# Kernel tuning notes

Hardware: AMD Instinct MI355X
Metric: run time of the kernel (lower is better)

Reference implementation:

```python
import jax, jax.numpy as jnp
import numpy as np

B, S, H, F, E, K = 2, 2048, 1024, 4096, 8, 2


def setup_inputs() -> dict:
    key = jax.random.key(0)
    ks = jax.random.split(key, 5)
    scale = 0.02
    return {
        "hidden_states": jax.random.normal(ks[0], (B, S, H), jnp.float32),
        "gate_w": jax.random.normal(ks[1], (H, E), jnp.float32) * scale,  # nn.Linear(H,E,bias=False)
        "w1": jax.random.normal(ks[2], (E, H, F), jnp.float32) * scale,   # per-expert fc1
        "b1": jnp.zeros((E, F), jnp.float32),
        "w2": jax.random.normal(ks[3], (E, F, H), jnp.float32) * scale,   # per-expert fc2
        "b2": jnp.zeros((E, H), jnp.float32),
    }


def reference(hidden_states, gate_w, w1, b1, w2, b2):
    b, s, h = hidden_states.shape
    x = hidden_states.reshape(b * s, h)  # [T, H]
    T = x.shape[0]
    n_experts = gate_w.shape[1]

    # --- Top-K gating ---
    router_logits = x @ gate_w                      # [T, E]
    router_probs = jax.nn.softmax(router_logits, axis=-1)
    topk_probs, topk_idx = jax.lax.top_k(router_probs, K)  # [T, K]
    topk_probs = topk_probs / topk_probs.sum(axis=-1, keepdims=True)
    aux_loss = n_experts * jnp.sum(router_probs.mean(axis=0) ** 2)

    # --- Combine weights: scatter normalized top-k probs into dense [T, E] ---
    combine_w = jnp.zeros((T, n_experts), x.dtype).at[
        jnp.arange(T)[:, None], topk_idx
    ].add(topk_probs)

    # --- Expert MLPs (dense per-expert batched GEMM; zero combine weight drops unrouted) ---
    hidden = jax.nn.relu(jnp.einsum('th,ehf->etf', x, w1) + b1[:, None, :])  # [E, T, F]
    expert_out = jnp.einsum('etf,efh->eth', hidden, w2) + b2[:, None, :]     # [E, T, H]

    out = jnp.einsum('te,eth->th', combine_w, expert_out)  # weighted combine
    return out.reshape(b, s, h), aux_loss
```

## Files before the change

kernel.cpp:

```cpp
#include <hip/hip_runtime.h>
#include <hip/hip_bf16.h>
#include <cstdint>

#define AS1 __attribute__((address_space(1)))
#define AS3 __attribute__((address_space(3)))

typedef __attribute__((ext_vector_type(8))) short short8x;
typedef __attribute__((ext_vector_type(4))) float f32x4;

static constexpr int T    = 4096;
static constexpr int HD   = 1024;
static constexpr int FD   = 4096;
static constexpr int NE   = 8;
static constexpr int P    = T * 2;
static constexpr int PPAD = P + 128;
static constexpr int MAXT = P / 128 + NE;
static constexpr int RTB  = 16;
static constexpr int RNB  = T / RTB;

static constexpr int TW1G = (FD / 64) * (HD / 64) * NE;
static constexpr int CVTG = (T * HD) / 1024;
static constexpr int FC1G = (FD / 128) * MAXT;
static constexpr int TW2G = (HD / 64) * (FD / 64) * NE;

struct TileDesc { int e; int start; int rows; int pad; };

__device__ __forceinline__ uint16_t f2bf(float f) {
  uint32_t u = __builtin_bit_cast(uint32_t, f);
  u += 0x7FFFu + ((u >> 16) & 1u);
  return (uint16_t)(u >> 16);
}
__device__ __forceinline__ float bf2f(uint16_t b) {
  uint32_t u = ((uint32_t)b) << 16;
  return __builtin_bit_cast(float, u);
}
__device__ __forceinline__ void gload_lds16(const void* g, void* l) {
  __builtin_amdgcn_global_load_lds((const AS1 uint32_t*)g, (AS3 uint32_t*)l, 16, 0, 0);
}

__device__ __forceinline__ void transpose_role(
    const float* __restrict__ in, uint16_t* __restrict__ out,
    int R, int C, int bi, float* tile ) {
  int nbc = C / 64;
  int nbr = R / 64;
  int cx = bi % nbc;
  int ry = (bi / nbc) % nbr;
  int z  = bi / (nbc * nbr);
  const float* inp = in + (size_t)z * R * C;
  uint16_t* outp = out + (size_t)z * R * C;
  int r0 = ry * 64, c0 = cx * 64;
  int tid = threadIdx.x;
  int lr = tid >> 4;
  int lc4 = (tid & 15) * 4;
#pragma unroll
  for (int p = 0; p < 4; ++p) {
    float4 v = *(const float4*)&inp[(size_t)(r0 + lr + p * 16) * C + c0 + lc4];
    tile[(lr + p * 16) * 65 + lc4 + 0] = v.x;
    tile[(lr + p * 16) * 65 + lc4 + 1] = v.y;
    tile[(lr + p * 16) * 65 + lc4 + 2] = v.z;
    tile[(lr + p * 16) * 65 + lc4 + 3] = v.w;
  }
  __syncthreads();
#pragma unroll
  for (int p = 0; p < 4; ++p) {
    int c = lr + p * 16;
    ushort4 o;
    o.x = f2bf(tile[(lc4 + 0) * 65 + c]);
    o.y = f2bf(tile[(lc4 + 1) * 65 + c]);
    o.z = f2bf(tile[(lc4 + 2) * 65 + c]);
    o.w = f2bf(tile[(lc4 + 3) * 65 + c]);
    *(ushort4*)&outp[(size_t)(c0 + c) * R + r0 + lc4] = o;
  }
}

__device__ __forceinline__ void cvt_role(const float* __restrict__ x,
                                         uint16_t* __restrict__ xb, int bi) {
  size_t i = ((size_t)bi * 256 + threadIdx.x) * 4;
  float4 v = *(const float4*)&x[i];
  ushort4 o;
  o.x = f2bf(v.x); o.y = f2bf(v.y); o.z = f2bf(v.z); o.w = f2bf(v.w);
  *(ushort4*)&xb[i] = o;
}

__device__ __forceinline__ void router_role(
    const float* __restrict__ x, const float* __restrict__ gate_w,
    int* __restrict__ topk_idx, float* __restrict__ topk_w,
    float* __restrict__ part_sums, int* __restrict__ part_counts,
    int rb, char* smem) {
  float* g  = (float*)smem;
  float* ls = (float*)(smem + 32768);
  int*   lc = (int*)(smem + 32768 + 32);
  int tid = threadIdx.x;
  for (int i = tid; i < NE * HD; i += 256)
    g[(i & 7) * HD + (i >> 3)] = gate_w[i];
  if (tid < NE) { ls[tid] = 0.f; lc[tid] = 0; }
  __syncthreads();
  int wave = tid >> 6, lane = tid & 63;
  float psum[NE];
#pragma unroll
  for (int e = 0; e < NE; ++e) psum[e] = 0.f;

  for (int tt = 0; tt < RTB / 4; ++tt) {
    int t = rb * RTB + wave * (RTB / 4) + tt;
    const float* xr = x + (size_t)t * HD;
    float acc[NE];
#pragma unroll
    for (int e = 0; e < NE; ++e) acc[e] = 0.f;
    for (int i = 0; i < HD / 64; ++i) {
      float xv = xr[lane + i * 64];
#pragma unroll
      for (int e = 0; e < NE; ++e) acc[e] += xv * g[e * HD + lane + i * 64];
    }
#pragma unroll
    for (int off = 32; off > 0; off >>= 1)
#pragma unroll
      for (int e = 0; e < NE; ++e) acc[e] += __shfl_down(acc[e], off);
    if (lane == 0) {
      float m = acc[0];
#pragma unroll
      for (int e = 1; e < NE; ++e) m = fmaxf(m, acc[e]);
      float p[NE], s = 0.f;
#pragma unroll
      for (int e = 0; e < NE; ++e) { p[e] = expf(acc[e] - m); s += p[e]; }
      float inv = 1.f / s;
#pragma unroll
      for (int e = 0; e < NE; ++e) { p[e] *= inv; psum[e] += p[e]; }
      int i0 = 0;
#pragma unroll
      for (int e = 1; e < NE; ++e) if (p[e] > p[i0]) i0 = e;
      int i1 = (i0 == 0) ? 1 : 0;
#pragma unroll
      for (int e = 0; e < NE; ++e) if (e != i0 && e != i1 && p[e] > p[i1]) i1 = e;
      float wsum = p[i0] + p[i1];
      topk_idx[t * 2] = i0; topk_idx[t * 2 + 1] = i1;
      topk_w[t * 2] = p[i0] / wsum; topk_w[t * 2 + 1] = p[i1] / wsum;
      atomicAdd(&lc[i0], 1); atomicAdd(&lc[i1], 1);
    }
  }
  if (lane == 0)
#pragma unroll
    for (int e = 0; e < NE; ++e) atomicAdd(&ls[e], psum[e]);
  __syncthreads();
  if (tid < NE) {
    part_sums[rb * NE + tid]   = ls[tid];
    part_counts[rb * NE + tid] = lc[tid];
  }
}

__global__ __launch_bounds__(256) void prep_kernel(
    const float* __restrict__ x, const float* __restrict__ gate_w,
    const float* __restrict__ w1,
    uint16_t* __restrict__ xb, uint16_t* __restrict__ w1t,
    int* __restrict__ topk_idx, float* __restrict__ topk_w,
    float* __restrict__ part_sums, int* __restrict__ part_counts) {
  __shared__ __align__(16) char smem[33024];
  int b = blockIdx.x;
  if (b < TW1G) {
    transpose_role(w1, w1t, HD, FD, b, (float*)smem);
  } else if (b < TW1G + CVTG) {
    cvt_role(x, xb, b - TW1G);
  } else {
    router_role(x, gate_w, topk_idx, topk_w, part_sums, part_counts,
                b - TW1G - CVTG, smem);
  }
}

__global__ __launch_bounds__(64) void finalize_kernel(
    const int* __restrict__ part_counts, const float* __restrict__ part_sums,
    int* __restrict__ offsets, TileDesc* __restrict__ desc,
    int* __restrict__ ntiles, float* __restrict__ aux_out) {
  __shared__ int   csh[NE];
  __shared__ float ssh[NE];
  int tid = threadIdx.x;
  if (tid < NE) {
    int c = 0; float s = 0.f;
    for (int b = 0; b < RNB; ++b) {
      c += part_counts[b * NE + tid];
      s += part_sums[b * NE + tid];
    }
    csh[tid] = c; ssh[tid] = s;
  }
  __syncthreads();
  if (tid == 0) {
    int off = 0, nt = 0;
    for (int e = 0; e < NE; ++e) {
      offsets[e] = off;
      int c = csh[e];
      for (int i = 0; i < c; i += 128) {
        int rows = c - i; if (rows > 128) rows = 128;
        desc[nt].e = e; desc[nt].start = off + i; desc[nt].rows = rows; desc[nt].pad = 0;
        nt++;
      }
      off += c;
    }
    *ntiles = nt;
    float aux = 0.f;
    for (int e = 0; e < NE; ++e) {
      float mean = ssh[e] / (float)T;
      aux += mean * mean;
    }
    *aux_out = (float)NE * aux;
  }
}

__global__ __launch_bounds__(256) void scatter_kernel(
    const int* __restrict__ topk_idx, const int* __restrict__ offsets,
    int* __restrict__ fill, int* __restrict__ pair_tok, int* __restrict__ tok_pos) {
  int t = blockIdx.x * 256 + threadIdx.x;
  int lane = threadIdx.x & 63;
  unsigned long long below = (lane == 63) ? ~0ull >> 1
                                          : ((1ull << (lane + 1)) - 1) >> 1;
#pragma unroll
  for (int k = 0; k < 2; ++k) {
    int e = topk_idx[t * 2 + k];
    int pos = 0;
    for (int ex = 0; ex < NE; ++ex) {
      unsigned long long m = __ballot(e == ex);
      if (e == ex) {
        int leader = __ffsll((long long)m) - 1;
        int cnt = __popcll(m);
        int base = 0;
        if (lane == leader) base = atomicAdd(&fill[ex], cnt);
        base = __shfl(base, leader);
        pos = base + __popcll(m & below);
      }
    }
    int pp = offsets[e] + pos;
    pair_tok[pp] = t;
    tok_pos[t * 2 + k] = pp;
  }
}

template <int KD, int ND, int NBG, int EPI>
__device__ __forceinline__ void gemm_role(
    char* smem, int orig,
    const uint16_t* __restrict__ Abase, const int* __restrict__ pair_tok,
    const uint16_t* __restrict__ Bw, const float* __restrict__ bias,
    uint16_t* __restrict__ Cout, const TileDesc* __restrict__ desc,
    const int* __restrict__ ntiles) {
  constexpr int SM = MAXT / 8;

  int xcd = orig & 7, local = orig >> 3;
  int nbq = local / (SM * NBG);
  int rem = local % (SM * NBG);
  int mt  = xcd * SM + rem / NBG;
  int nb  = nbq * NBG + rem % NBG;
  if (mt >= *ntiles) return;
  TileDesc d = desc[mt];

  uint16_t* As = (uint16_t*)smem;
  uint16_t* Bs = (uint16_t*)(smem + 8192);
  int* rowA    = (int*)(smem + 16384);

  int tid = threadIdx.x, lane = tid & 63, wave = tid >> 6;
  int wm = wave >> 1, wn = wave & 1;

  int idx0 = (wave * 2 + 0) * 64 + lane;
  int idx1 = (wave * 2 + 1) * 64 + lane;
  int ar0 = idx0 >> 2, kc0 = idx0 & 3;
  int ar1 = idx1 >> 2, kc1 = idx1 & 3;

  int ra0, ra1;
  if constexpr (EPI == 0) {
    if (tid < 128) rowA[tid] = (tid < d.rows) ? pair_tok[d.start + tid] : 0;
    __syncthreads();
    ra0 = rowA[ar0]; ra1 = rowA[ar1];
  } else {
    ra0 = d.start + ar0; ra1 = d.start + ar1;
  }

  const uint16_t* Bbase = Bw + ((size_t)d.e * ND + (size_t)nb * 128) * KD;

  f32x4 acc[4][4];
#pragma unroll
  for (int i = 0; i < 4; ++i)
#pragma unroll
    for (int j = 0; j < 4; ++j) acc[i][j] = (f32x4){0.f, 0.f, 0.f, 0.f};

  for (int kt = 0; kt < KD / 32; ++kt) {
    if (kt) __syncthreads();
    int kb = kt * 32;
    gload_lds16(Abase + (size_t)ra0 * KD + kb + kc0 * 8, &As[(wave * 2 + 0) * 512]);
    gload_lds16(Abase + (size_t)ra1 * KD + kb + kc1 * 8, &As[(wave * 2 + 1) * 512]);
    gload_lds16(Bbase + (size_t)ar0 * KD + kb + kc0 * 8, &Bs[(wave * 2 + 0) * 512]);
    gload_lds16(Bbase + (size_t)ar1 * KD + kb + kc1 * 8, &Bs[(wave * 2 + 1) * 512]);
    __syncthreads();

    short8x af[4], bfr[4];
#pragma unroll
    for (int i = 0; i < 4; ++i)
      af[i] = *(const short8x*)&As[(wm * 64 + i * 16 + (lane & 15)) * 32 + (lane >> 4) * 8];
#pragma unroll
    for (int j = 0; j < 4; ++j)
      bfr[j] = *(const short8x*)&Bs[(wn * 64 + j * 16 + (lane & 15)) * 32 + (lane >> 4) * 8];
#pragma unroll
    for (int i = 0; i < 4; ++i)
#pragma unroll
      for (int j = 0; j < 4; ++j)
        acc[i][j] = __builtin_amdgcn_mfma_f32_16x16x32_bf16(af[i], bfr[j], acc[i][j], 0, 0, 0);
  }

  int rq = (lane >> 4) * 4;
  int cl = lane & 15;
#pragma unroll
  for (int i = 0; i < 4; ++i) {
    int rb = wm * 64 + i * 16 + rq;
#pragma unroll
    for (int j = 0; j < 4; ++j) {
      int col = nb * 128 + wn * 64 + j * 16 + cl;
      float bv = bias[d.e * ND + col];
#pragma unroll
      for (int q = 0; q < 4; ++q) {
        int r = rb + q;
        if (r < d.rows) {
          float v = acc[i][j][q] + bv;
          if (EPI == 0) v = fmaxf(v, 0.f);
          Cout[(size_t)(d.start + r) * ND + col] = f2bf(v);
        }
      }
    }
  }
}

__global__ __launch_bounds__(256) void fc1_fused_kernel(
    const uint16_t* __restrict__ xb, const int* __restrict__ pair_tok,
    const uint16_t* __restrict__ w1t, const float* __restrict__ b1,
    uint16_t* __restrict__ hidden, const TileDesc* __restrict__ desc,
    const int* __restrict__ ntiles,
    const float* __restrict__ w2, uint16_t* __restrict__ w2t) {
  __shared__ __align__(16) char smem[17408];
  int b = blockIdx.x;
  if (b < FC1G) {
    gemm_role<HD, FD, 4, 0>(smem, b, xb, pair_tok, w1t, b1, hidden, desc, ntiles);
  } else {
    transpose_role(w2, w2t, FD, HD, b - FC1G, (float*)smem);
  }
}

__global__ __launch_bounds__(256) void fc2_kernel(
    const uint16_t* __restrict__ hidden, const uint16_t* __restrict__ w2t,
    const float* __restrict__ b2, uint16_t* __restrict__ pout,
    const TileDesc* __restrict__ desc, const int* __restrict__ ntiles) {
  __shared__ __align__(16) char smem[17408];
  gemm_role<FD, HD, 8, 1>(smem, blockIdx.x, hidden, nullptr, w2t, b2, pout, desc, ntiles);
}

__global__ __launch_bounds__(256) void combine_kernel(
    const uint16_t* __restrict__ po, const int* __restrict__ tok_pos,
    const float* __restrict__ topk_w, float* __restrict__ out) {
  int t = blockIdx.x;
  int c = threadIdx.x * 4;
  int p0 = tok_pos[t * 2], p1 = tok_pos[t * 2 + 1];
  float w0 = topk_w[t * 2], w1 = topk_w[t * 2 + 1];
  ushort4 a = *(const ushort4*)&po[(size_t)p0 * HD + c];
  ushort4 b = *(const ushort4*)&po[(size_t)p1 * HD + c];
  float4 o;
  o.x = w0 * bf2f(a.x) + w1 * bf2f(b.x);
  o.y = w0 * bf2f(a.y) + w1 * bf2f(b.y);
  o.z = w0 * bf2f(a.z) + w1 * bf2f(b.z);
  o.w = w0 * bf2f(a.w) + w1 * bf2f(b.w);
  *(float4*)&out[(size_t)t * HD + c] = o;
}

extern "C" void kernel_launch(void* const* d_in, const int* in_sizes, int n_in,
                              void* d_out, int out_size, void* d_ws, size_t ws_size,
                              hipStream_t stream) {
  const float* x      = (const float*)d_in[0];
  const float* gate_w = (const float*)d_in[1];
  const float* w1     = (const float*)d_in[2];
  const float* b1     = (const float*)d_in[3];
  const float* w2     = (const float*)d_in[4];
  const float* b2     = (const float*)d_in[5];
  float* out = (float*)d_out;
  (void)in_sizes; (void)n_in; (void)out_size; (void)ws_size;

  char* w = (char*)d_ws;
  size_t off = 0;
  auto alloc = [&](size_t bytes) -> void* {
    void* p = w + off;
    off = (off + bytes + 255) & ~(size_t)255;
    return p;
  };
  int*      meta     = (int*)alloc(256);
  int*      fill     = meta;
  int*      offsets  = (int*)alloc(256);
  int*      ntiles   = offsets + 8;
  TileDesc* desc     = (TileDesc*)alloc(sizeof(TileDesc) * 128);
  int*      topk_idx = (int*)alloc(sizeof(int) * P);
  float*    topk_w   = (float*)alloc(sizeof(float) * P);
  int*      tok_pos  = (int*)alloc(sizeof(int) * P);
  int*      pair_tok = (int*)alloc(sizeof(int) * PPAD);
  float*    psums    = (float*)alloc(sizeof(float) * RNB * NE);
  int*      pcounts  = (int*)alloc(sizeof(int) * RNB * NE);
  uint16_t* xb       = (uint16_t*)alloc((size_t)T * HD * 2);
  uint16_t* w1t      = (uint16_t*)alloc((size_t)NE * FD * HD * 2);
  uint16_t* w2t      = (uint16_t*)alloc((size_t)NE * HD * FD * 2);
  uint16_t* hidden   = (uint16_t*)alloc((size_t)PPAD * FD * 2);
  uint16_t* pout     = (uint16_t*)alloc((size_t)PPAD * HD * 2);

  hipMemsetAsync(meta, 0, 256, stream);
  prep_kernel<<<TW1G + CVTG + RNB, 256, 0, stream>>>(
      x, gate_w, w1, xb, w1t, topk_idx, topk_w, psums, pcounts);
  finalize_kernel<<<1, 64, 0, stream>>>(pcounts, psums, offsets, desc, ntiles,
                                        out + (size_t)T * HD);
  scatter_kernel<<<T / 256, 256, 0, stream>>>(topk_idx, offsets, fill, pair_tok, tok_pos);
  fc1_fused_kernel<<<FC1G + TW2G, 256, 0, stream>>>(
      xb, pair_tok, w1t, b1, hidden, desc, ntiles, w2, w2t);
  fc2_kernel<<<(HD / 128) * MAXT, 256, 0, stream>>>(
      hidden, w2t, b2, pout, desc, ntiles);
  combine_kernel<<<T, 256, 0, stream>>>(pout, tok_pos, topk_w, out);
}
```

Before: 377.6 us.

## Fuse weighted combine into fc2 epilogue via atomic adds; read gate weights directly

The fc2 GEMM epilogue now scales each output row by its routing weight and atomically adds it into the zeroed fp32 output at the token's row. This removes the bf16 pair-output buffer and the separate combine kernel, and the scatter kernel writes per-pair weights instead of token positions. The router also stops staging the gate matrix in shared memory and reads it straight from global memory as float4s, which halves prep_kernel's LDS use. In exchange the output must be memset every call, the epilogue issues scalar float atomics, and the order of the two-way sum becomes nondeterministic.

```diff
diff --git a/kernel.cpp b/kernel.cpp
--- a/kernel.cpp
+++ b/kernel.cpp
@@ -87,12 +87,9 @@
     int* __restrict__ topk_idx, float* __restrict__ topk_w,
     float* __restrict__ part_sums, int* __restrict__ part_counts,
     int rb, char* smem) {
-  float* g  = (float*)smem;
-  float* ls = (float*)(smem + 32768);
-  int*   lc = (int*)(smem + 32768 + 32);
+  float* ls = (float*)smem;
+  int*   lc = (int*)(smem + 32);
   int tid = threadIdx.x;
-  for (int i = tid; i < NE * HD; i += 256)
-    g[(i & 7) * HD + (i >> 3)] = gate_w[i];
   if (tid < NE) { ls[tid] = 0.f; lc[tid] = 0; }
   __syncthreads();
   int wave = tid >> 6, lane = tid & 63;
@@ -107,9 +104,14 @@
 #pragma unroll
     for (int e = 0; e < NE; ++e) acc[e] = 0.f;
     for (int i = 0; i < HD / 64; ++i) {
-      float xv = xr[lane + i * 64];
-#pragma unroll
-      for (int e = 0; e < NE; ++e) acc[e] += xv * g[e * HD + lane + i * 64];
+      int h = lane + i * 64;
+      float xv = xr[h];
+      float4 g0 = *(const float4*)&gate_w[(size_t)h * 8];
+      float4 g1 = *(const float4*)&gate_w[(size_t)h * 8 + 4];
+      acc[0] += xv * g0.x; acc[1] += xv * g0.y;
+      acc[2] += xv * g0.z; acc[3] += xv * g0.w;
+      acc[4] += xv * g1.x; acc[5] += xv * g1.y;
+      acc[6] += xv * g1.z; acc[7] += xv * g1.w;
     }
 #pragma unroll
     for (int off = 32; off > 0; off >>= 1)
@@ -153,7 +155,7 @@
     uint16_t* __restrict__ xb, uint16_t* __restrict__ w1t,
     int* __restrict__ topk_idx, float* __restrict__ topk_w,
     float* __restrict__ part_sums, int* __restrict__ part_counts) {
-  __shared__ __align__(16) char smem[33024];
+  __shared__ __align__(16) char smem[16640];
   int b = blockIdx.x;
   if (b < TW1G) {
     transpose_role(w1, w1t, HD, FD, b, (float*)smem);
@@ -204,8 +206,9 @@
 }
 
 __global__ __launch_bounds__(256) void scatter_kernel(
-    const int* __restrict__ topk_idx, const int* __restrict__ offsets,
-    int* __restrict__ fill, int* __restrict__ pair_tok, int* __restrict__ tok_pos) {
+    const int* __restrict__ topk_idx, const float* __restrict__ topk_w,
+    const int* __restrict__ offsets, int* __restrict__ fill,
+    int* __restrict__ pair_tok, float* __restrict__ pair_w) {
   int t = blockIdx.x * 256 + threadIdx.x;
   int lane = threadIdx.x & 63;
   unsigned long long below = (lane == 63) ? ~0ull >> 1
@@ -227,7 +230,7 @@
     }
     int pp = offsets[e] + pos;
     pair_tok[pp] = t;
-    tok_pos[t * 2 + k] = pp;
+    pair_w[pp]   = topk_w[t * 2 + k];
   }
 }
 
@@ -235,9 +238,10 @@
 __device__ __forceinline__ void gemm_role(
     char* smem, int orig,
     const uint16_t* __restrict__ Abase, const int* __restrict__ pair_tok,
+    const float* __restrict__ pair_w,
     const uint16_t* __restrict__ Bw, const float* __restrict__ bias,
-    uint16_t* __restrict__ Cout, const TileDesc* __restrict__ desc,
-    const int* __restrict__ ntiles) {
+    uint16_t* __restrict__ Cout, float* __restrict__ outA,
+    const TileDesc* __restrict__ desc, const int* __restrict__ ntiles) {
   constexpr int SM = MAXT / 8;
 
   int xcd = orig & 7, local = orig >> 3;
@@ -250,7 +254,8 @@
 
   uint16_t* As = (uint16_t*)smem;
   uint16_t* Bs = (uint16_t*)(smem + 8192);
-  int* rowA    = (int*)(smem + 16384);
+  int*   rowA  = (int*)(smem + 16384);
+  float* rowW  = (float*)(smem + 16896);
 
   int tid = threadIdx.x, lane = tid & 63, wave = tid >> 6;
   int wm = wave >> 1, wn = wave & 1;
@@ -266,6 +271,11 @@
     __syncthreads();
     ra0 = rowA[ar0]; ra1 = rowA[ar1];
   } else {
+    if (tid < 128) {
+      rowA[tid] = (tid < d.rows) ? pair_tok[d.start + tid] : 0;
+      rowW[tid] = (tid < d.rows) ? pair_w[d.start + tid] : 0.f;
+    }
+    __syncthreads();
     ra0 = d.start + ar0; ra1 = d.start + ar1;
   }
 
@@ -314,8 +324,12 @@
         int r = rb + q;
         if (r < d.rows) {
           float v = acc[i][j][q] + bv;
-          if (EPI == 0) v = fmaxf(v, 0.f);
-          Cout[(size_t)(d.start + r) * ND + col] = f2bf(v);
+          if constexpr (EPI == 0) {
+            v = fmaxf(v, 0.f);
+            Cout[(size_t)(d.start + r) * ND + col] = f2bf(v);
+          } else {
+            unsafeAtomicAdd(&outA[(size_t)rowA[r] * ND + col], rowW[r] * v);
+          }
         }
       }
     }
@@ -331,35 +345,21 @@
   __shared__ __align__(16) char smem[17408];
   int b = blockIdx.x;
   if (b < FC1G) {
-    gemm_role<HD, FD, 4, 0>(smem, b, xb, pair_tok, w1t, b1, hidden, desc, ntiles);
+    gemm_role<HD, FD, 4, 0>(smem, b, xb, pair_tok, nullptr, w1t, b1,
+                            hidden, nullptr, desc, ntiles);
   } else {
     transpose_role(w2, w2t, FD, HD, b - FC1G, (float*)smem);
   }
 }
 
 __global__ __launch_bounds__(256) void fc2_kernel(
-    const uint16_t* __restrict__ hidden, const uint16_t* __restrict__ w2t,
-    const float* __restrict__ b2, uint16_t* __restrict__ pout,
+    const uint16_t* __restrict__ hidden, const int* __restrict__ pair_tok,
+    const float* __restrict__ pair_w, const uint16_t* __restrict__ w2t,
+    const float* __restrict__ b2, float* __restrict__ out,
     const TileDesc* __restrict__ desc, const int* __restrict__ ntiles) {
   __shared__ __align__(16) char smem[17408];
-  gemm_role<FD, HD, 8, 1>(smem, blockIdx.x, hidden, nullptr, w2t, b2, pout, desc, ntiles);
-}
-
-__global__ __launch_bounds__(256) void combine_kernel(
-    const uint16_t* __restrict__ po, const int* __restrict__ tok_pos,
-    const float* __restrict__ topk_w, float* __restrict__ out) {
-  int t = blockIdx.x;
-  int c = threadIdx.x * 4;
-  int p0 = tok_pos[t * 2], p1 = tok_pos[t * 2 + 1];
-  float w0 = topk_w[t * 2], w1 = topk_w[t * 2 + 1];
-  ushort4 a = *(const ushort4*)&po[(size_t)p0 * HD + c];
-  ushort4 b = *(const ushort4*)&po[(size_t)p1 * HD + c];
-  float4 o;
-  o.x = w0 * bf2f(a.x) + w1 * bf2f(b.x);
-  o.y = w0 * bf2f(a.y) + w1 * bf2f(b.y);
-  o.z = w0 * bf2f(a.z) + w1 * bf2f(b.z);
-  o.w = w0 * bf2f(a.w) + w1 * bf2f(b.w);
-  *(float4*)&out[(size_t)t * HD + c] = o;
+  gemm_role<FD, HD, 8, 1>(smem, blockIdx.x, hidden, pair_tok, pair_w, w2t, b2,
+                          nullptr, out, desc, ntiles);
 }
 
 extern "C" void kernel_launch(void* const* d_in, const int* in_sizes, int n_in,
@@ -388,25 +388,25 @@
   TileDesc* desc     = (TileDesc*)alloc(sizeof(TileDesc) * 128);
   int*      topk_idx = (int*)alloc(sizeof(int) * P);
   float*    topk_w   = (float*)alloc(sizeof(float) * P);
-  int*      tok_pos  = (int*)alloc(sizeof(int) * P);
   int*      pair_tok = (int*)alloc(sizeof(int) * PPAD);
+  float*    pair_w   = (float*)alloc(sizeof(float) * PPAD);
   float*    psums    = (float*)alloc(sizeof(float) * RNB * NE);
   int*      pcounts  = (int*)alloc(sizeof(int) * RNB * NE);
   uint16_t* xb       = (uint16_t*)alloc((size_t)T * HD * 2);
   uint16_t* w1t      = (uint16_t*)alloc((size_t)NE * FD * HD * 2);
   uint16_t* w2t      = (uint16_t*)alloc((size_t)NE * HD * FD * 2);
   uint16_t* hidden   = (uint16_t*)alloc((size_t)PPAD * FD * 2);
-  uint16_t* pout     = (uint16_t*)alloc((size_t)PPAD * HD * 2);
 
   hipMemsetAsync(meta, 0, 256, stream);
+  hipMemsetAsync(out, 0, (size_t)T * HD * sizeof(float), stream);
   prep_kernel<<<TW1G + CVTG + RNB, 256, 0, stream>>>(
       x, gate_w, w1, xb, w1t, topk_idx, topk_w, psums, pcounts);
   finalize_kernel<<<1, 64, 0, stream>>>(pcounts, psums, offsets, desc, ntiles,
                                         out + (size_t)T * HD);
-  scatter_kernel<<<T / 256, 256, 0, stream>>>(topk_idx, offsets, fill, pair_tok, tok_pos);
+  scatter_kernel<<<T / 256, 256, 0, stream>>>(topk_idx, topk_w, offsets, fill,
+                                              pair_tok, pair_w);
   fc1_fused_kernel<<<FC1G + TW2G, 256, 0, stream>>>(
       xb, pair_tok, w1t, b1, hidden, desc, ntiles, w2, w2t);
   fc2_kernel<<<(HD / 128) * MAXT, 256, 0, stream>>>(
-      hidden, w2t, b2, pout, desc, ntiles);
-  combine_kernel<<<T, 256, 0, stream>>>(pout, tok_pos, topk_w, out);
-}
+      hidden, pair_tok, pair_w, w2t, b2, out, desc, ntiles);
+}
```

New measurement: 402.3 us. 1.07x slower.
